# Performance work log

Hardware: AMD Instinct MI355X
Metric: run time of the kernel (lower is better)

Reference implementation:

```python
import jax, jax.numpy as jnp
import numpy as np

N_NODES = 100000
N_EDGES = 1600000
IN_F, HID_F, OUT_F = 128, 128, 128


def setup_inputs() -> dict:
    key = jax.random.key(0)
    ks = jax.random.split(key, 12)
    x = jax.random.normal(ks[0], (N_NODES, IN_F), dtype=jnp.float32)
    src = jax.random.randint(ks[1], (N_EDGES,), 0, N_NODES)
    dst = jax.random.randint(ks[2], (N_EDGES,), 0, N_NODES)
    s = 1.0 / np.sqrt(IN_F)
    W1_self = jax.random.uniform(ks[3], (HID_F, IN_F), minval=-s, maxval=s)
    W1_neigh = jax.random.uniform(ks[4], (HID_F, IN_F), minval=-s, maxval=s)
    b1 = jnp.zeros((HID_F,), jnp.float32)
    s2 = 1.0 / np.sqrt(HID_F)
    W2_self = jax.random.uniform(ks[5], (OUT_F, HID_F), minval=-s2, maxval=s2)
    W2_neigh = jax.random.uniform(ks[6], (OUT_F, HID_F), minval=-s2, maxval=s2)
    b2 = jnp.zeros((OUT_F,), jnp.float32)
    s3 = 1.0 / np.sqrt(OUT_F)
    W3 = jax.random.uniform(ks[7], (OUT_F, OUT_F), minval=-s3, maxval=s3)
    b3 = jax.random.uniform(ks[8], (OUT_F,), minval=-s3, maxval=s3)
    return {"x": x, "src": src, "dst": dst,
            "W1_self": W1_self, "W1_neigh": W1_neigh, "b1": b1,
            "W2_self": W2_self, "W2_neigh": W2_neigh, "b2": b2,
            "W3": W3, "b3": b3}


def _sage_conv(h, src, dst, W_self, W_neigh, b):
    # DGL SAGEConv 'mean': h_neigh = mean over in-neighbors (src -> dst)
    msg = h[src]  # [E, d] irregular gather
    summed = jax.ops.segment_sum(msg, dst, num_segments=N_NODES)  # [N, d]
    deg = jax.ops.segment_sum(jnp.ones((src.shape[0],), h.dtype), dst,
                              num_segments=N_NODES)
    h_neigh = summed / jnp.clip(deg, 1.0)[:, None]
    return h @ W_self.T + h_neigh @ W_neigh.T + b


def reference(x, src, dst, W1_self, W1_neigh, b1, W2_self, W2_neigh, b2, W3, b3):
    h = _sage_conv(x, src, dst, W1_self, W1_neigh, b1)
    h = jax.nn.relu(h)
    h = _sage_conv(h, src, dst, W2_self, W2_neigh, b2)
    return h @ W3.T + b3
```

## Files before the change

kernel.cpp:

```cpp
#include <hip/hip_runtime.h>

#define N_NODES 100000
#define N_EDGES 1600000
#define F 128
#define NB_SCAN ((N_NODES + 1023) / 1024)
#define NSUB 32
#define SUB_NODES (N_NODES / NSUB)
#define BCAP 128
#define PCAP 65536
#define NCVT ((N_NODES * F / 8 + 255) / 256)
#define BUCKET_BLOCKS 512
#define PREP_BLOCKS (NCVT + 257)

typedef short short8 __attribute__((ext_vector_type(8)));
typedef float f32x4 __attribute__((ext_vector_type(4)));
typedef unsigned short ushort_t;
typedef ushort_t ushort8 __attribute__((ext_vector_type(8)));

__device__ __forceinline__ ushort_t f2b(float f) {
    union { float f; unsigned u; } v; v.f = f;
    unsigned r = v.u + 0x7fff + ((v.u >> 16) & 1);
    return (ushort_t)(r >> 16);
}


__global__ __launch_bounds__(256) void k_bucket_prep(
        const int* __restrict__ src, const int* __restrict__ dst,
        int2* __restrict__ pairs, int* __restrict__ gcur,
        const float* __restrict__ x, ushort_t* __restrict__ xb,
        const float* __restrict__ W1s, const float* __restrict__ W1n,
        const float* __restrict__ W2s, const float* __restrict__ W2n,
        const float* __restrict__ W3, const float* __restrict__ b2,
        const float* __restrict__ b3,
        ushort_t* __restrict__ wb, float* __restrict__ bc) {
    const int tid = threadIdx.x;

    if (blockIdx.x >= BUCKET_BLOCKS) {
        const int blk = blockIdx.x - BUCKET_BLOCKS;
        if (blk < NCVT) {
            int i = blk * 256 + tid;
            if (i >= N_NODES * F / 8) return;
            const float4* p = reinterpret_cast<const float4*>(x) + (size_t)i * 2;
            float4 a = p[0], b = p[1];
            ushort8 r;
            r[0] = f2b(a.x); r[1] = f2b(a.y); r[2] = f2b(a.z); r[3] = f2b(a.w);
            r[4] = f2b(b.x); r[5] = f2b(b.y); r[6] = f2b(b.z); r[7] = f2b(b.w);
            *reinterpret_cast<ushort8*>(xb + (size_t)i * 8) = r;
            return;
        }
        const int b = blk - NCVT;
        if (b < 128) {
            int g = b * 256 + tid;
            float v = (g < F * F) ? W1s[g] : W1n[g - F * F];
            wb[g] = f2b(v);
        } else if (b < 256) {
            int g = (b - 128) * 256 + tid;
            int m = g >> 14, rem = g & 16383, i = rem >> 7, j = rem & 127;
            const float* __restrict__ W2 = m ? W2n : W2s;
            float s = 0.f;
#pragma unroll 8
            for (int k = 0; k < F; ++k) s += W3[i * F + k] * W2[k * F + j];
            wb[2 * F * F + g] = f2b(s);
        } else if (tid < F) {
            float s = b3[tid];
#pragma unroll 8
            for (int k = 0; k < F; ++k) s += W3[tid * F + k] * b2[k];
            bc[tid] = s;
        }
        return;
    }

    __shared__ int2 lbuf[NSUB * BCAP];
    __shared__ int lcnt[NSUB], fbase[NSUB], fcnt[NSUB];
    if (tid < NSUB) lcnt[tid] = 0;
    __syncthreads();

    for (int base = blockIdx.x * 1024; base < N_EDGES; base += BUCKET_BLOCKS * 1024) {
#pragma unroll
        for (int r = 0; r < 4; ++r) {
            int idx = base + r * 256 + tid;
            if (idx < N_EDGES) {
                int d = dst[idx], s = src[idx];
                int p = d / SUB_NODES;
                int dl = d - p * SUB_NODES;
                int slot = atomicAdd(&lcnt[p], 1);
                if (slot < BCAP) lbuf[p * BCAP + slot] = make_int2(dl, s);
                else {
                    int g = atomicAdd(&gcur[p], 1);
                    pairs[(size_t)p * PCAP + g] = make_int2(dl, s);
                }
            }
        }
        __syncthreads();
        if (tid < NSUB) {
            int c = lcnt[tid]; if (c > BCAP) c = BCAP;
            fcnt[tid] = c;
            fbase[tid] = atomicAdd(&gcur[tid], c);
        }
        __syncthreads();
        for (int p = 0; p < NSUB; ++p) {
            int c = fcnt[p];
            for (int i = tid; i < c; i += 256)
                pairs[(size_t)p * PCAP + fbase[p] + i] = lbuf[p * BCAP + i];
        }
        __syncthreads();
        if (tid < NSUB) lcnt[tid] = 0;
        __syncthreads();
    }
}

__global__ __launch_bounds__(1024) void k_histb(const int2* __restrict__ pairs,
                                                const int* __restrict__ gcur,
                                                int* __restrict__ cnt) {
    __shared__ int hc[SUB_NODES];
    const int p = blockIdx.x;
    for (int i = threadIdx.x; i < SUB_NODES; i += 1024) hc[i] = 0;
    __syncthreads();
    const int n = gcur[p];
    const int2* __restrict__ sl = pairs + (size_t)p * PCAP;
    for (int i = threadIdx.x; i < n; i += 1024) atomicAdd(&hc[sl[i].x], 1);
    __syncthreads();
    for (int i = threadIdx.x; i < SUB_NODES; i += 1024)
        cnt[p * SUB_NODES + i] = hc[i];
}

__global__ __launch_bounds__(1024) void k_scan1(const int* __restrict__ cnt,
                                                int* __restrict__ tmp,
                                                int* __restrict__ bsum) {
    __shared__ int ws[16];
    const int t = threadIdx.x, lane = t & 63, w = t >> 6;
    const int gid = blockIdx.x * 1024 + t;
    int v = (gid < N_NODES) ? cnt[gid] : 0;
    int x = v;
#pragma unroll
    for (int off = 1; off < 64; off <<= 1) {
        int y = __shfl_up(x, off, 64);
        if (lane >= off) x += y;
    }
    if (lane == 63) ws[w] = x;
    __syncthreads();
    if (w == 0) {
        int s = (lane < 16) ? ws[lane] : 0;
#pragma unroll
        for (int off = 1; off < 16; off <<= 1) {
            int y = __shfl_up(s, off, 64);
            if (lane >= off) s += y;
        }
        if (lane < 16) ws[lane] = s;
    }
    __syncthreads();
    int base = (w == 0) ? 0 : ws[w - 1];
    int incl = base + x;
    if (gid < N_NODES) tmp[gid] = incl;
    if (t == 1023) bsum[blockIdx.x] = incl;
}

__global__ __launch_bounds__(256) void k_scan23(const int* __restrict__ tmp,
                                                const int* __restrict__ bsum,
                                                int* __restrict__ row_ptr) {
    __shared__ int excl[NB_SCAN];
    const int t = threadIdx.x;
    if (t < 64) {
        const int lane = t;
        int v0 = (lane < NB_SCAN) ? bsum[lane] : 0;
        int v1 = (64 + lane < NB_SCAN) ? bsum[64 + lane] : 0;
        int x0 = v0;
#pragma unroll
        for (int off = 1; off < 64; off <<= 1) {
            int y = __shfl_up(x0, off, 64);
            if (lane >= off) x0 += y;
        }
        int tot0 = __shfl(x0, 63, 64);
        int x1 = v1;
#pragma unroll
        for (int off = 1; off < 64; off <<= 1) {
            int y = __shfl_up(x1, off, 64);
            if (lane >= off) x1 += y;
        }
        if (lane < NB_SCAN) excl[lane] = x0 - v0;
        if (64 + lane < NB_SCAN) excl[64 + lane] = tot0 + x1 - v1;
    }
    __syncthreads();
    int gid = blockIdx.x * 256 + t;
    if (gid >= N_NODES) return;
    row_ptr[gid + 1] = excl[gid >> 10] + tmp[gid];
    if (gid == 0) row_ptr[0] = 0;
}

__global__ __launch_bounds__(1024) void k_place(const int2* __restrict__ pairs,
                                                const int* __restrict__ gcur,
                                                const int* __restrict__ row_ptr,
                                                int* __restrict__ col) {
    __shared__ int cur[SUB_NODES];
    const int p = blockIdx.x;
    for (int i = threadIdx.x; i < SUB_NODES; i += 1024)
        cur[i] = row_ptr[p * SUB_NODES + i];
    __syncthreads();
    const int n = gcur[p];
    const int2* __restrict__ sl = pairs + (size_t)p * PCAP;
    for (int i = threadIdx.x; i < n; i += 1024) {
        int2 pr = sl[i];
        int pos = atomicAdd(&cur[pr.x], 1);
        col[pos] = pr.y;
    }
}


__global__ __launch_bounds__(256) void k_agg(const ushort_t* __restrict__ h,
                                             const int* __restrict__ row_ptr,
                                             const int* __restrict__ col,
                                             ushort_t* __restrict__ out) {
    int node = (blockIdx.x * blockDim.x + threadIdx.x) >> 6;
    if (node >= N_NODES) return;
    const int lane = threadIdx.x & 63;
    const unsigned loff = (unsigned)lane * 4u;
    const char* __restrict__ hb = reinterpret_cast<const char*>(h);
    const int beg = row_ptr[node], end = row_ptr[node + 1];
    float ax = 0.f, ay = 0.f;
    for (int e = beg; e < end; e += 8) {
        unsigned v[8];
#pragma unroll
        for (int u = 0; u < 8; ++u) {
            int idx = e + u; idx = (idx < end) ? idx : end - 1;
            unsigned s = (unsigned)col[idx];
            v[u] = *reinterpret_cast<const unsigned*>(hb + (size_t)((s << 8) + loff));
        }
#pragma unroll
        for (int u = 0; u < 8; ++u) {
            unsigned vv = (e + u < end) ? v[u] : 0u;
            ax += __uint_as_float(vv << 16);
            ay += __uint_as_float(vv & 0xffff0000u);
        }
    }
    int deg = end - beg;
    float inv = 1.0f / (float)(deg > 0 ? deg : 1);
    unsigned r = ((unsigned)f2b(ax * inv)) | (((unsigned)f2b(ay * inv)) << 16);
    *reinterpret_cast<unsigned*>(out + ((size_t)node << 7) + lane * 2) = r;
}


template <bool RELU, bool F32OUT>
__global__ __launch_bounds__(512) void k_layer(
        const ushort_t* __restrict__ A0, const ushort_t* __restrict__ A1,
        const ushort_t* __restrict__ W0, const ushort_t* __restrict__ W1,
        const float* __restrict__ bias, void* __restrict__ outv) {
    const int t = threadIdx.x;
    const int lane = t & 63;
    const int wid = t >> 6;
    const int wr = wid >> 2;
    const int wc = wid & 3;
    const int node0 = blockIdx.x * 128;
    const int arow = lane & 15;
    const int kgrp = lane >> 4;

    f32x4 acc[4][2];
#pragma unroll
    for (int fr = 0; fr < 4; ++fr)
#pragma unroll
        for (int fc = 0; fc < 2; ++fc) acc[fr][fc] = (f32x4)(0.f);

#pragma unroll
    for (int ph = 0; ph < 2; ++ph) {
        const ushort_t* __restrict__ A = ph ? A1 : A0;
        const ushort_t* __restrict__ W = ph ? W1 : W0;

        short8 bfrag[4][2];
#pragma unroll
        for (int ks = 0; ks < 4; ++ks)
#pragma unroll
            for (int fc = 0; fc < 2; ++fc) {
                int c = wc * 32 + fc * 16 + arow;
                bfrag[ks][fc] = *reinterpret_cast<const short8*>(W + c * F + ks * 32 + kgrp * 8);
            }

#pragma unroll
        for (int ks = 0; ks < 4; ++ks) {
            short8 afrag[4];
#pragma unroll
            for (int fr = 0; fr < 4; ++fr) {
                int r = node0 + wr * 64 + fr * 16 + arow;
                if (r > N_NODES - 1) r = N_NODES - 1;
                afrag[fr] = *reinterpret_cast<const short8*>(A + (size_t)r * F + ks * 32 + kgrp * 8);
            }
#pragma unroll
            for (int fr = 0; fr < 4; ++fr)
#pragma unroll
                for (int fc = 0; fc < 2; ++fc)
                    acc[fr][fc] = __builtin_amdgcn_mfma_f32_16x16x32_bf16(
                        afrag[fr], bfrag[ks][fc], acc[fr][fc], 0, 0, 0);
        }
    }

#pragma unroll
    for (int fr = 0; fr < 4; ++fr)
#pragma unroll
        for (int fc = 0; fc < 2; ++fc) {
            int c = wc * 32 + fc * 16 + (lane & 15);
            float bv = bias[c];
#pragma unroll
            for (int r4 = 0; r4 < 4; ++r4) {
                int row = node0 + wr * 64 + fr * 16 + (lane >> 4) * 4 + r4;
                if (row >= N_NODES) continue;
                float v = acc[fr][fc][r4] + bv;
                if (RELU) v = fmaxf(v, 0.f);
                if (F32OUT)
                    reinterpret_cast<float*>(outv)[(size_t)row * F + c] = v;
                else
                    reinterpret_cast<ushort_t*>(outv)[(size_t)row * F + c] = f2b(v);
            }
        }
}


extern "C" void kernel_launch(void* const* d_in, const int* in_sizes, int n_in,
                              void* d_out, int out_size, void* d_ws, size_t ws_size,
                              hipStream_t stream) {
    const float* x   = (const float*)d_in[0];
    const int*   src = (const int*)d_in[1];
    const int*   dst = (const int*)d_in[2];
    const float* W1s = (const float*)d_in[3];
    const float* W1n = (const float*)d_in[4];
    const float* b1  = (const float*)d_in[5];
    const float* W2s = (const float*)d_in[6];
    const float* W2n = (const float*)d_in[7];
    const float* b2  = (const float*)d_in[8];
    const float* W3  = (const float*)d_in[9];
    const float* b3  = (const float*)d_in[10];
    float* out = (float*)d_out;

    char* p = (char*)d_ws;
    auto align512 = [](size_t v) { return (v + 511) & ~(size_t)511; };
    int* row_ptr = (int*)p;        p += align512((N_NODES + 1) * sizeof(int));
    int* cnt     = (int*)p;        p += align512((size_t)N_NODES * sizeof(int));
    int* stmp    = (int*)p;        p += align512((size_t)N_NODES * sizeof(int));
    int* bsum    = (int*)p;        p += align512(256 * sizeof(int));
    int* gcur    = (int*)p;        p += align512(NSUB * sizeof(int));
    int* col     = (int*)p;        p += align512((size_t)N_EDGES * sizeof(int));
    ushort_t* wb = (ushort_t*)p;   p += align512((size_t)4 * F * F * sizeof(ushort_t));
    float* bc    = (float*)p;      p += align512(F * sizeof(float));
    ushort_t* xb = (ushort_t*)p;   p += align512((size_t)N_NODES * F * sizeof(ushort_t));
    ushort_t* aggb = (ushort_t*)p; p += align512((size_t)N_NODES * F * sizeof(ushort_t));
    ushort_t* h1b  = (ushort_t*)p; p += align512((size_t)N_NODES * F * sizeof(ushort_t));
    int2* pairs = (int2*)aggb;

    hipMemsetAsync(gcur, 0, NSUB * sizeof(int), stream);
    k_bucket_prep<<<BUCKET_BLOCKS + PREP_BLOCKS, 256, 0, stream>>>(
        src, dst, pairs, gcur, x, xb, W1s, W1n, W2s, W2n, W3, b2, b3, wb, bc);
    k_histb<<<NSUB, 1024, 0, stream>>>(pairs, gcur, cnt);
    k_scan1<<<NB_SCAN, 1024, 0, stream>>>(cnt, stmp, bsum);
    k_scan23<<<(N_NODES + 255) / 256, 256, 0, stream>>>(stmp, bsum, row_ptr);
    k_place<<<NSUB, 1024, 0, stream>>>(pairs, gcur, row_ptr, col);

    const int agg_grid = (N_NODES + 3) / 4;
    const int gemm_grid = (N_NODES + 127) / 128;

    k_agg<<<agg_grid, 256, 0, stream>>>(xb, row_ptr, col, aggb);
    k_layer<true, false><<<gemm_grid, 512, 0, stream>>>(
        xb, aggb, wb + 0 * F * F, wb + 1 * F * F, b1, h1b);

    k_agg<<<agg_grid, 256, 0, stream>>>(h1b, row_ptr, col, aggb);
    k_layer<false, true><<<gemm_grid, 512, 0, stream>>>(
        h1b, aggb, wb + 2 * F * F, wb + 3 * F * F, bc, out);
}
```

Baseline: 324.8 us.

## Split per-bucket histogram and placement across chunks for more blocks

The histogram and CSR placement kernels previously ran one 1024-thread block per destination bucket, only 32 blocks, which leaves most compute units idle. Each bucket's edge list is now split into 8 chunks, each handled by its own block that writes a private histogram. The scan sums the chunk histograms, and placement offsets each chunk's cursor by the counts of the earlier chunks. This adds extra histogram traffic, stored in the h1b buffer before it is used, and the placement within a node stays nondeterministic as before.

```diff
diff --git a/kernel.cpp b/kernel.cpp
--- a/kernel.cpp
+++ b/kernel.cpp
@@ -8,6 +8,7 @@
 #define SUB_NODES (N_NODES / NSUB)
 #define BCAP 128
 #define PCAP 65536
+#define NCHUNK 8
 #define NCVT ((N_NODES * F / 8 + 255) / 256)
 #define BUCKET_BLOCKS 512
 #define PREP_BLOCKS (NCVT + 257)
@@ -109,28 +110,38 @@
     }
 }
 
-__global__ __launch_bounds__(1024) void k_histb(const int2* __restrict__ pairs,
+__global__ __launch_bounds__(1024) void k_histc(const int2* __restrict__ pairs,
                                                 const int* __restrict__ gcur,
-                                                int* __restrict__ cnt) {
+                                                int* __restrict__ hists) {
     __shared__ int hc[SUB_NODES];
-    const int p = blockIdx.x;
+    const int p = blockIdx.x / NCHUNK;
+    const int c = blockIdx.x % NCHUNK;
     for (int i = threadIdx.x; i < SUB_NODES; i += 1024) hc[i] = 0;
     __syncthreads();
     const int n = gcur[p];
+    const int chunk = (n + NCHUNK - 1) / NCHUNK;
+    const int lo = c * chunk;
+    int hi = lo + chunk; if (hi > n) hi = n;
     const int2* __restrict__ sl = pairs + (size_t)p * PCAP;
-    for (int i = threadIdx.x; i < n; i += 1024) atomicAdd(&hc[sl[i].x], 1);
-    __syncthreads();
-    for (int i = threadIdx.x; i < SUB_NODES; i += 1024)
-        cnt[p * SUB_NODES + i] = hc[i];
-}
-
-__global__ __launch_bounds__(1024) void k_scan1(const int* __restrict__ cnt,
+    for (int i = lo + threadIdx.x; i < hi; i += 1024) atomicAdd(&hc[sl[i].x], 1);
+    __syncthreads();
+    int* __restrict__ hout = hists + ((size_t)p * NCHUNK + c) * SUB_NODES;
+    for (int i = threadIdx.x; i < SUB_NODES; i += 1024) hout[i] = hc[i];
+}
+
+__global__ __launch_bounds__(1024) void k_scan1(const int* __restrict__ hists,
                                                 int* __restrict__ tmp,
                                                 int* __restrict__ bsum) {
     __shared__ int ws[16];
     const int t = threadIdx.x, lane = t & 63, w = t >> 6;
     const int gid = blockIdx.x * 1024 + t;
-    int v = (gid < N_NODES) ? cnt[gid] : 0;
+    int v = 0;
+    if (gid < N_NODES) {
+        int p = gid / SUB_NODES, i = gid - p * SUB_NODES;
+        const int* __restrict__ hp = hists + (size_t)p * NCHUNK * SUB_NODES + i;
+#pragma unroll
+        for (int c = 0; c < NCHUNK; ++c) v += hp[c * SUB_NODES];
+    }
     int x = v;
 #pragma unroll
     for (int off = 1; off < 64; off <<= 1) {
@@ -187,18 +198,27 @@
     if (gid == 0) row_ptr[0] = 0;
 }
 
-__global__ __launch_bounds__(1024) void k_place(const int2* __restrict__ pairs,
-                                                const int* __restrict__ gcur,
-                                                const int* __restrict__ row_ptr,
-                                                int* __restrict__ col) {
+__global__ __launch_bounds__(1024) void k_place2(const int2* __restrict__ pairs,
+                                                 const int* __restrict__ gcur,
+                                                 const int* __restrict__ row_ptr,
+                                                 const int* __restrict__ hists,
+                                                 int* __restrict__ col) {
     __shared__ int cur[SUB_NODES];
-    const int p = blockIdx.x;
-    for (int i = threadIdx.x; i < SUB_NODES; i += 1024)
-        cur[i] = row_ptr[p * SUB_NODES + i];
+    const int p = blockIdx.x / NCHUNK;
+    const int c = blockIdx.x % NCHUNK;
+    const int* __restrict__ hp = hists + (size_t)p * NCHUNK * SUB_NODES;
+    for (int i = threadIdx.x; i < SUB_NODES; i += 1024) {
+        int s = row_ptr[p * SUB_NODES + i];
+        for (int cc = 0; cc < c; ++cc) s += hp[cc * SUB_NODES + i];
+        cur[i] = s;
+    }
     __syncthreads();
     const int n = gcur[p];
+    const int chunk = (n + NCHUNK - 1) / NCHUNK;
+    const int lo = c * chunk;
+    int hi = lo + chunk; if (hi > n) hi = n;
     const int2* __restrict__ sl = pairs + (size_t)p * PCAP;
-    for (int i = threadIdx.x; i < n; i += 1024) {
+    for (int i = lo + threadIdx.x; i < hi; i += 1024) {
         int2 pr = sl[i];
         int pos = atomicAdd(&cur[pr.x], 1);
         col[pos] = pr.y;
@@ -331,7 +351,6 @@
     char* p = (char*)d_ws;
     auto align512 = [](size_t v) { return (v + 511) & ~(size_t)511; };
     int* row_ptr = (int*)p;        p += align512((N_NODES + 1) * sizeof(int));
-    int* cnt     = (int*)p;        p += align512((size_t)N_NODES * sizeof(int));
     int* stmp    = (int*)p;        p += align512((size_t)N_NODES * sizeof(int));
     int* bsum    = (int*)p;        p += align512(256 * sizeof(int));
     int* gcur    = (int*)p;        p += align512(NSUB * sizeof(int));
@@ -342,14 +361,15 @@
     ushort_t* aggb = (ushort_t*)p; p += align512((size_t)N_NODES * F * sizeof(ushort_t));
     ushort_t* h1b  = (ushort_t*)p; p += align512((size_t)N_NODES * F * sizeof(ushort_t));
     int2* pairs = (int2*)aggb;
+    int* hists = (int*)h1b;
 
     hipMemsetAsync(gcur, 0, NSUB * sizeof(int), stream);
     k_bucket_prep<<<BUCKET_BLOCKS + PREP_BLOCKS, 256, 0, stream>>>(
         src, dst, pairs, gcur, x, xb, W1s, W1n, W2s, W2n, W3, b2, b3, wb, bc);
-    k_histb<<<NSUB, 1024, 0, stream>>>(pairs, gcur, cnt);
-    k_scan1<<<NB_SCAN, 1024, 0, stream>>>(cnt, stmp, bsum);
+    k_histc<<<NSUB * NCHUNK, 1024, 0, stream>>>(pairs, gcur, hists);
+    k_scan1<<<NB_SCAN, 1024, 0, stream>>>(hists, stmp, bsum);
     k_scan23<<<(N_NODES + 255) / 256, 256, 0, stream>>>(stmp, bsum, row_ptr);
-    k_place<<<NSUB, 1024, 0, stream>>>(pairs, gcur, row_ptr, col);
+    k_place2<<<NSUB * NCHUNK, 1024, 0, stream>>>(pairs, gcur, row_ptr, hists, col);
 
     const int agg_grid = (N_NODES + 3) / 4;
     const int gemm_grid = (N_NODES + 127) / 128;
```

New measurement: 302.0 us. 7.0% less time.
